# Performance work log

Measured on AMD Instinct MI355X. Metric: run time of the kernel, lower is better.

## Reference

```python
import jax, jax.numpy as jnp
import numpy as np

D_MODEL = 1024

def setup_inputs() -> dict:
    key = jax.random.key(0)
    kx, kq, kk, kv, ko = jax.random.split(key, 5)
    B, S, D = 8, 2048, D_MODEL
    scale = 1.0 / np.sqrt(D)
    x = jax.random.normal(kx, (B, S, D), dtype=jnp.float32)
    # nn.Linear weights are [out, in]; y = x @ W.T
    Wq = jax.random.normal(kq, (D, D), dtype=jnp.float32) * scale
    Wk = jax.random.normal(kk, (D, D), dtype=jnp.float32) * scale
    Wv = jax.random.normal(kv, (D, D), dtype=jnp.float32) * scale
    Wo = jax.random.normal(ko, (D, D), dtype=jnp.float32) * scale
    return {"x": x, "Wq": Wq, "Wk": Wk, "Wv": Wv, "Wo": Wo}

def reference(x, Wq, Wk, Wv, Wo):
    # Single-head self-attention, dropout in eval mode (identity).
    d_model = x.shape[-1]
    q = jnp.einsum('bsd,ed->bse', x, Wq)
    k = jnp.einsum('bsd,ed->bse', x, Wk)
    v = jnp.einsum('bsd,ed->bse', x, Wv)
    scores = jnp.einsum('bqe,bke->bqk', q, k) / jnp.sqrt(jnp.float32(d_model))
    attn = jax.nn.softmax(scores, axis=-1)
    weighted = jnp.einsum('bqk,bke->bqe', attn, v)
    return jnp.einsum('bqe,oe->bqo', weighted, Wo)
```

## Files before the change

kernel.cpp:

```cpp
#include <hip/hip_runtime.h>
#include <hip/hip_bf16.h>
#include <stdint.h>

typedef short bf16x8 __attribute__((ext_vector_type(8)));
typedef float f32x4 __attribute__((ext_vector_type(4)));

__device__ __forceinline__ unsigned short f2bf(float x) {
  uint32_t u = __builtin_bit_cast(uint32_t, x);
  u += 0x7FFFu + ((u >> 16) & 1u);
  return (unsigned short)(u >> 16);
}
__device__ __forceinline__ float bf2f(unsigned short u) {
  uint32_t v = ((uint32_t)u) << 16;
  return __builtin_bit_cast(float, v);
}

__device__ __forceinline__ void gl2lds16(const void* g, void* l) {
  __builtin_amdgcn_global_load_lds(
      (const __attribute__((address_space(1))) unsigned int*)g,
      (__attribute__((address_space(3))) unsigned int*)l, 16, 0, 0);
}

__global__ __launch_bounds__(256) void cast_f32_bf16_k(
    const float* __restrict__ s, unsigned short* __restrict__ d, long n) {
  long i = ((long)blockIdx.x * 256 + threadIdx.x) * 8;
  if (i >= n) return;
  float4 a = *(const float4*)(s + i);
  float4 b = *(const float4*)(s + i + 4);
  bf16x8 o;
  o[0] = (short)f2bf(a.x); o[1] = (short)f2bf(a.y);
  o[2] = (short)f2bf(a.z); o[3] = (short)f2bf(a.w);
  o[4] = (short)f2bf(b.x); o[5] = (short)f2bf(b.y);
  o[6] = (short)f2bf(b.z); o[7] = (short)f2bf(b.w);
  *(bf16x8*)(d + i) = o;
}

__global__ __launch_bounds__(256) void cast4_f32_bf16_k(
    const float* __restrict__ s0, const float* __restrict__ s1,
    const float* __restrict__ s2, const float* __restrict__ s3,
    unsigned short* __restrict__ d, long n) {
  const float* s = blockIdx.z == 0 ? s0 : blockIdx.z == 1 ? s1 : blockIdx.z == 2 ? s2 : s3;
  long i = ((long)blockIdx.x * 256 + threadIdx.x) * 8;
  if (i >= n) return;
  float4 a = *(const float4*)(s + i);
  float4 b = *(const float4*)(s + i + 4);
  bf16x8 o;
  o[0] = (short)f2bf(a.x); o[1] = (short)f2bf(a.y);
  o[2] = (short)f2bf(a.z); o[3] = (short)f2bf(a.w);
  o[4] = (short)f2bf(b.x); o[5] = (short)f2bf(b.y);
  o[6] = (short)f2bf(b.z); o[7] = (short)f2bf(b.w);
  *(bf16x8*)(d + blockIdx.z * n + i) = o;
}

template <typename OutT, bool FUSEQKV>
__global__ __launch_bounds__(512, 2) void gemm_bt8(
    const unsigned short* __restrict__ A, const unsigned short* __restrict__ B,
    OutT* __restrict__ C, int M, int N, int K,
    long sA, long sB, long sC, float alpha) {
  extern __shared__ __align__(16) char smem[];
  const int bz = blockIdx.z;
  const int gx = gridDim.x;
  const int nwg = gx * gridDim.y;
  const int idx = blockIdx.y * gx + blockIdx.x;
  const int wg = (idx & 7) * (nwg >> 3) + (idx >> 3);
  const int bm = wg / gx, bn = wg % gx;

  const int tid = threadIdx.x, lane = tid & 63, wave = tid >> 6;
  const int wm = wave >> 2, wn = wave & 3;

  const char* Ac = (const char*)(A + (long)bz * sA + (long)bm * 256 * K);
  const char* Bc = (const char*)(B + (long)bz * sB + (long)bn * 256 * K);
  C += (long)bz * sC;
  const long ld = (long)K * 2;

  const int sr = tid >> 3;
  const int scol = (((tid & 7) ^ ((tid >> 3) & 7)) << 4);

  auto stageChunk = [&](int buf, int op, int c, const char* gbase, int ktb) {
    char* reg = smem + ((buf * 2 + op) << 15);
    gl2lds16(gbase + (long)(sr + c * 64) * ld + (ktb + scol),
             reg + c * 8192 + tid * 16);
  };

  const int colx0 = ((lane >> 4) << 4) ^ ((lane & 7) << 4);
  const int colx1 = (64 | ((lane >> 4) << 4)) ^ ((lane & 7) << 4);
  const int rbA = (wm * 128 + (lane & 15)) * 128;
  const int rbB = (wn * 64 + (lane & 15)) * 128;

  f32x4 acc[8][4] = {};
  bf16x8 a0[4], a1[4], b0[4], b1[4];

  auto rdA = [&](bf16x8* dst, const char* reg, int g, int colx) {
#pragma unroll
    for (int m = 0; m < 4; ++m)
      dst[m] = *(const bf16x8*)(reg + rbA + g * (64 * 128) + m * (16 * 128) + colx);
  };
  auto rdB = [&](bf16x8* dst, const char* reg, int colx) {
#pragma unroll
    for (int n = 0; n < 4; ++n)
      dst[n] = *(const bf16x8*)(reg + rbB + n * (16 * 128) + colx);
  };
  auto mfma16 = [&](const bf16x8* af, const bf16x8* bf_, int g) {
    __builtin_amdgcn_s_setprio(1);
#pragma unroll
    for (int m = 0; m < 4; ++m)
#pragma unroll
      for (int n = 0; n < 4; ++n)
        acc[g * 4 + m][n] = __builtin_amdgcn_mfma_f32_16x16x32_bf16(
            af[m], bf_[n], acc[g * 4 + m][n], 0, 0, 0);
    __builtin_amdgcn_s_setprio(0);
    __builtin_amdgcn_sched_barrier(0);
  };

#pragma unroll
  for (int c = 0; c < 4; ++c) stageChunk(0, 0, c, Ac, 0);
#pragma unroll
  for (int c = 0; c < 4; ++c) stageChunk(0, 1, c, Bc, 0);
  asm volatile("s_waitcnt vmcnt(0)" ::: "memory");
  __builtin_amdgcn_s_barrier();
  rdA(a0, smem, 0, colx0);
  rdB(b0, smem + (1 << 15), colx0);

  const int nt = K >> 6;
  for (int t = 0; t < nt; ++t) {
    const int b = t & 1;
    const bool pf = (t + 1 < nt);
    const int ktb = (t + 1) << 7;
    const char* regA0 = smem + ((b * 2 + 0) << 15);
    const char* regB0 = smem + ((b * 2 + 1) << 15);
    const char* regA1 = smem + (((b ^ 1) * 2 + 0) << 15);
    const char* regB1 = smem + (((b ^ 1) * 2 + 1) << 15);

    if (pf) {
#pragma unroll
      for (int c = 0; c < 4; ++c) stageChunk(b ^ 1, 0, c, Ac, ktb);
    }
    rdA(a1, regA0, 1, colx0);
    asm volatile("s_waitcnt lgkmcnt(4)" ::: "memory");
    __builtin_amdgcn_sched_barrier(0);
    mfma16(a0, b0, 0);
    __builtin_amdgcn_s_barrier();

    if (pf) {
#pragma unroll
      for (int c = 0; c < 4; ++c) stageChunk(b ^ 1, 1, c, Bc, ktb);
    }
    rdA(a0, regA0, 0, colx1);
    rdB(b1, regB0, colx1);
    asm volatile("s_waitcnt lgkmcnt(8)" ::: "memory");
    __builtin_amdgcn_sched_barrier(0);
    mfma16(a1, b0, 1);
    __builtin_amdgcn_s_barrier();

    rdA(a1, regA0, 1, colx1);
    asm volatile("s_waitcnt lgkmcnt(4)" ::: "memory");
    __builtin_amdgcn_sched_barrier(0);
    mfma16(a0, b1, 0);
    __builtin_amdgcn_s_barrier();

    if (pf) {
      asm volatile("s_waitcnt vmcnt(0)" ::: "memory");
      __builtin_amdgcn_s_barrier();
      rdA(a0, regA1, 0, colx0);
      rdB(b0, regB1, colx0);
      asm volatile("s_waitcnt lgkmcnt(8)" ::: "memory");
    } else {
      asm volatile("s_waitcnt lgkmcnt(0)" ::: "memory");
    }
    __builtin_amdgcn_sched_barrier(0);
    mfma16(a1, b1, 1);
    __builtin_amdgcn_s_barrier();
  }

  const long row0 = (long)bm * 256 + wm * 128 + (lane >> 4) * 4;
  const int col0 = bn * 256 + wn * 64 + (lane & 15);
  if constexpr (FUSEQKV) {
    const int tensor = bn >> 2;
    unsigned short* dst = (unsigned short*)C + ((long)tensor << 24);
    const int colb0 = col0 - (tensor << 10);
#pragma unroll
    for (int m = 0; m < 8; ++m) {
#pragma unroll
      for (int n = 0; n < 4; ++n) {
        if (tensor < 2) {
#pragma unroll
          for (int r = 0; r < 4; ++r)
            dst[(row0 + m * 16 + r) * 1024 + colb0 + n * 16] = f2bf(acc[m][n][r]);
        } else {
          long row = row0 + m * 16;
          long base = ((row >> 11) << 21) + ((long)(colb0 + n * 16) << 11) + (row & 2047);
          ushort4 st;
          st.x = f2bf(acc[m][n][0]); st.y = f2bf(acc[m][n][1]);
          st.z = f2bf(acc[m][n][2]); st.w = f2bf(acc[m][n][3]);
          *(ushort4*)(dst + base) = st;
        }
      }
    }
  } else {
#pragma unroll
    for (int m = 0; m < 8; ++m) {
#pragma unroll
      for (int n = 0; n < 4; ++n) {
#pragma unroll
        for (int r = 0; r < 4; ++r) {
          long row = row0 + m * 16 + r;
          int col = col0 + n * 16;
          float v = acc[m][n][r] * alpha;
          if constexpr (sizeof(OutT) == 2)
            C[row * (long)N + col] = (OutT)f2bf(v);
          else
            C[row * (long)N + col] = v;
        }
      }
    }
  }
}

__global__ __launch_bounds__(256) void softmax_inplace(unsigned short* __restrict__ s, int C) {
  __shared__ float red[8];
  long row = blockIdx.x;
  unsigned short* p = s + row * (long)C;
  int tid = threadIdx.x, lane = tid & 63, w = tid >> 6;
  bf16x8 raw = *(const bf16x8*)(p + tid * 8);
  float v[8];
  float mx = -3.4e38f;
#pragma unroll
  for (int j = 0; j < 8; ++j) { v[j] = bf2f((unsigned short)raw[j]); mx = fmaxf(mx, v[j]); }
#pragma unroll
  for (int o = 32; o > 0; o >>= 1) mx = fmaxf(mx, __shfl_xor(mx, o));
  if (lane == 0) red[w] = mx;
  __syncthreads();
  mx = fmaxf(fmaxf(red[0], red[1]), fmaxf(red[2], red[3]));
  float sum = 0.f;
#pragma unroll
  for (int j = 0; j < 8; ++j) { v[j] = __expf(v[j] - mx); sum += v[j]; }
#pragma unroll
  for (int o = 32; o > 0; o >>= 1) sum += __shfl_xor(sum, o);
  if (lane == 0) red[4 + w] = sum;
  __syncthreads();
  float inv = 1.f / (red[4] + red[5] + red[6] + red[7]);
  bf16x8 o8;
#pragma unroll
  for (int j = 0; j < 8; ++j) o8[j] = (short)f2bf(v[j] * inv);
  *(bf16x8*)(p + tid * 8) = o8;
}

extern "C" void kernel_launch(void* const* d_in, const int* in_sizes, int n_in,
                              void* d_out, int out_size, void* d_ws, size_t ws_size,
                              hipStream_t stream) {
  (void)in_sizes; (void)n_in; (void)out_size; (void)ws_size;
  const float* x  = (const float*)d_in[0];
  const float* Wq = (const float*)d_in[1];
  const float* Wk = (const float*)d_in[2];
  const float* Wv = (const float*)d_in[3];
  const float* Wo = (const float*)d_in[4];
  const int B = 8, S = 2048, D = 1024;
  const long MB = 1 << 20;
  char* w = (char*)d_ws;
  unsigned short* Wqb = (unsigned short*)(w + 0 * MB);
  unsigned short* Wob = (unsigned short*)(w + 6 * MB);
  unsigned short* xb  = (unsigned short*)(w + 8 * MB);
  unsigned short* qb  = (unsigned short*)(w + 40 * MB);
  unsigned short* kb  = (unsigned short*)(w + 72 * MB);
  unsigned short* vt  = (unsigned short*)(w + 104 * MB);
  unsigned short* wb  = xb;
  unsigned short* attn = (unsigned short*)d_out;
  float* out = (float*)d_out;

  long nx = (long)B * S * D;
  long nw = (long)D * D;

  const int LDSB = 131072;
  hipFuncSetAttribute((const void*)gemm_bt8<unsigned short, true>,
                      hipFuncAttributeMaxDynamicSharedMemorySize, LDSB);
  hipFuncSetAttribute((const void*)gemm_bt8<unsigned short, false>,
                      hipFuncAttributeMaxDynamicSharedMemorySize, LDSB);
  hipFuncSetAttribute((const void*)gemm_bt8<float, false>,
                      hipFuncAttributeMaxDynamicSharedMemorySize, LDSB);

  cast_f32_bf16_k<<<(int)(nx / 2048), 256, 0, stream>>>(x, xb, nx);
  dim3 gW((int)(nw / 2048), 1, 4);
  cast4_f32_bf16_k<<<gW, 256, 0, stream>>>(Wq, Wk, Wv, Wo, Wqb, nw);

  dim3 gF(3072 / 256, (B * S) / 256, 1);
  gemm_bt8<unsigned short, true><<<gF, 512, LDSB, stream>>>(
      xb, Wqb, qb, B * S, 3072, D, 0, 0, 0, 1.f);

  dim3 gS(S / 256, S / 256, B);
  gemm_bt8<unsigned short, false><<<gS, 512, LDSB, stream>>>(qb, kb, attn, S, S, D,
      (long)S * D, (long)S * D, (long)S * S, 0.03125f);

  softmax_inplace<<<B * S, 256, 0, stream>>>(attn, S);

  dim3 gPV(D / 256, S / 256, B);
  gemm_bt8<unsigned short, false><<<gPV, 512, LDSB, stream>>>(attn, vt, wb, S, D, S,
      (long)S * S, (long)D * S, (long)S * D, 1.f);

  dim3 gP(D / 256, (B * S) / 256, 1);
  gemm_bt8<float, false><<<gP, 512, LDSB, stream>>>(wb, Wob, out, B * S, D, D, 0, 0, 0, 1.f);
}
```

Baseline: 324.4 us.

## Restructure GEMM main loop into half-tile staged pipeline with interleaved prefetch

Reorganizes the 256x256 bf16 GEMM k-loop so shared memory is split into 16KB half-tiles per operand and buffer. Global-to-LDS loads of the next A and B halves are issued piecemeal inside the MFMA sub-steps, with vmcnt(4) waits instead of full drains. The loop is unrolled two k-tiles at a time, and each wave reads smaller A and B fragments per sub-step. The aim is to overlap global loads with MFMA more evenly and shorten stalls, at the cost of more barriers and finer-grained synchronization that is harder to get right.

```diff
diff --git a/kernel.cpp b/kernel.cpp
--- a/kernel.cpp
+++ b/kernel.cpp
@@ -73,103 +73,86 @@
   C += (long)bz * sC;
   const long ld = (long)K * 2;
 
-  const int sr = tid >> 3;
-  const int scol = (((tid & 7) ^ ((tid >> 3) & 7)) << 4);
-
-  auto stageChunk = [&](int buf, int op, int c, const char* gbase, int ktb) {
-    char* reg = smem + ((buf * 2 + op) << 15);
-    gl2lds16(gbase + (long)(sr + c * 64) * ld + (ktb + scol),
-             reg + c * 8192 + tid * 16);
+  const int sr8 = tid >> 3;
+  const int scolx = (((tid & 7) ^ ((tid >> 3) & 7)) << 4);
+
+  auto stageHalf = [&](int t, int op, int h, const char* gbase) {
+    char* reg = smem + (((((t & 1) << 1) | op) << 1 | h) << 14);
+    const long ktb = (long)t << 7;
+#pragma unroll
+    for (int c = 0; c < 2; ++c)
+      gl2lds16(gbase + (long)(h * 128 + c * 64 + sr8) * ld + ktb + scolx,
+               reg + c * 8192 + tid * 16);
   };
 
-  const int colx0 = ((lane >> 4) << 4) ^ ((lane & 7) << 4);
-  const int colx1 = (64 | ((lane >> 4) << 4)) ^ ((lane & 7) << 4);
-  const int rbA = (wm * 128 + (lane & 15)) * 128;
-  const int rbB = (wn * 64 + (lane & 15)) * 128;
+  const char* Areg[2] = { smem + ((0 << 2 | wm) << 14),
+                          smem + ((1 << 2 | wm) << 14) };
+  const char* Breg[2] = { smem + (((0 << 2) | 2 | (wn >> 1)) << 14),
+                          smem + (((1 << 2) | 2 | (wn >> 1)) << 14) };
+  const int cko[2] = { (((lane >> 4) << 4) ^ ((lane & 7) << 4)),
+                       ((64 | ((lane >> 4) << 4)) ^ ((lane & 7) << 4)) };
+  const int rowA0 = (lane & 15) * 128;
+  const int rowB0 = ((wn & 1) * 64 + (lane & 15)) * 128;
 
   f32x4 acc[8][4] = {};
-  bf16x8 a0[4], a1[4], b0[4], b1[4];
-
-  auto rdA = [&](bf16x8* dst, const char* reg, int g, int colx) {
-#pragma unroll
-    for (int m = 0; m < 4; ++m)
-      dst[m] = *(const bf16x8*)(reg + rbA + g * (64 * 128) + m * (16 * 128) + colx);
-  };
-  auto rdB = [&](bf16x8* dst, const char* reg, int colx) {
-#pragma unroll
-    for (int n = 0; n < 4; ++n)
-      dst[n] = *(const bf16x8*)(reg + rbB + n * (16 * 128) + colx);
-  };
-  auto mfma16 = [&](const bf16x8* af, const bf16x8* bf_, int g) {
-    __builtin_amdgcn_s_setprio(1);
-#pragma unroll
-    for (int m = 0; m < 4; ++m)
-#pragma unroll
-      for (int n = 0; n < 4; ++n)
-        acc[g * 4 + m][n] = __builtin_amdgcn_mfma_f32_16x16x32_bf16(
-            af[m], bf_[n], acc[g * 4 + m][n], 0, 0, 0);
-    __builtin_amdgcn_s_setprio(0);
-    __builtin_amdgcn_sched_barrier(0);
-  };
-
-#pragma unroll
-  for (int c = 0; c < 4; ++c) stageChunk(0, 0, c, Ac, 0);
-#pragma unroll
-  for (int c = 0; c < 4; ++c) stageChunk(0, 1, c, Bc, 0);
-  asm volatile("s_waitcnt vmcnt(0)" ::: "memory");
+
+  stageHalf(0, 1, 0, Bc); stageHalf(0, 1, 1, Bc);
+  stageHalf(0, 0, 0, Ac); stageHalf(0, 0, 1, Ac);
+  stageHalf(1, 1, 0, Bc); stageHalf(1, 1, 1, Bc);
+  asm volatile("s_waitcnt vmcnt(4)" ::: "memory");
   __builtin_amdgcn_s_barrier();
-  rdA(a0, smem, 0, colx0);
-  rdB(b0, smem + (1 << 15), colx0);
 
   const int nt = K >> 6;
-  for (int t = 0; t < nt; ++t) {
-    const int b = t & 1;
-    const bool pf = (t + 1 < nt);
-    const int ktb = (t + 1) << 7;
-    const char* regA0 = smem + ((b * 2 + 0) << 15);
-    const char* regB0 = smem + ((b * 2 + 1) << 15);
-    const char* regA1 = smem + (((b ^ 1) * 2 + 0) << 15);
-    const char* regB1 = smem + (((b ^ 1) * 2 + 1) << 15);
-
-    if (pf) {
-#pragma unroll
-      for (int c = 0; c < 4; ++c) stageChunk(b ^ 1, 0, c, Ac, ktb);
+  const int niter = nt >> 1;
+  for (int i = 0; i < niter; ++i) {
+    const int u = 2 * i;
+    const bool pf = (i + 1 < niter);
+#pragma unroll
+    for (int d = 0; d < 2; ++d) {
+      bf16x8 b[4][2];
+#pragma unroll
+      for (int mq = 0; mq < 4; ++mq) {
+        bf16x8 a[2][2];
+        if (mq == 0) {
+#pragma unroll
+          for (int n = 0; n < 4; ++n)
+#pragma unroll
+            for (int kh = 0; kh < 2; ++kh)
+              b[n][kh] = *(const bf16x8*)(Breg[d] + rowB0 + n * 2048 + cko[kh]);
+        }
+#pragma unroll
+        for (int j = 0; j < 2; ++j)
+#pragma unroll
+          for (int kh = 0; kh < 2; ++kh)
+            a[j][kh] = *(const bf16x8*)(Areg[d] + rowA0 + (mq * 2 + j) * 2048 + cko[kh]);
+        if (d == 0 && mq == 0) { stageHalf(u + 1, 0, 0, Ac); stageHalf(u + 1, 0, 1, Ac); }
+        if (d == 0 && mq == 1 && pf) stageHalf(u + 2, 1, 0, Bc);
+        if (d == 0 && mq == 2 && pf) stageHalf(u + 2, 1, 1, Bc);
+        if (d == 1 && mq == 0 && pf) { stageHalf(u + 2, 0, 0, Ac); stageHalf(u + 2, 0, 1, Ac); }
+        if (d == 1 && mq == 1 && pf) stageHalf(u + 3, 1, 0, Bc);
+        if (d == 1 && mq == 2 && pf) stageHalf(u + 3, 1, 1, Bc);
+        if (mq == 0) asm volatile("s_waitcnt lgkmcnt(8)" ::: "memory");
+        __builtin_amdgcn_s_barrier();
+        asm volatile("s_waitcnt lgkmcnt(0)" ::: "memory");
+        __builtin_amdgcn_sched_barrier(0);
+        __builtin_amdgcn_s_setprio(1);
+#pragma unroll
+        for (int kh = 0; kh < 2; ++kh)
+#pragma unroll
+          for (int j = 0; j < 2; ++j)
+#pragma unroll
+            for (int n = 0; n < 4; ++n)
+              acc[mq * 2 + j][n] = __builtin_amdgcn_mfma_f32_16x16x32_bf16(
+                  a[j][kh], b[n][kh], acc[mq * 2 + j][n], 0, 0, 0);
+        __builtin_amdgcn_s_setprio(0);
+        if (d == 0 && mq == 3) {
+          if (pf) asm volatile("s_waitcnt vmcnt(4)" ::: "memory");
+          else    asm volatile("s_waitcnt vmcnt(0)" ::: "memory");
+        }
+        if (d == 1 && mq == 3 && pf) asm volatile("s_waitcnt vmcnt(4)" ::: "memory");
+        __builtin_amdgcn_s_barrier();
+      }
     }
-    rdA(a1, regA0, 1, colx0);
-    asm volatile("s_waitcnt lgkmcnt(4)" ::: "memory");
-    __builtin_amdgcn_sched_barrier(0);
-    mfma16(a0, b0, 0);
-    __builtin_amdgcn_s_barrier();
-
-    if (pf) {
-#pragma unroll
-      for (int c = 0; c < 4; ++c) stageChunk(b ^ 1, 1, c, Bc, ktb);
-    }
-    rdA(a0, regA0, 0, colx1);
-    rdB(b1, regB0, colx1);
-    asm volatile("s_waitcnt lgkmcnt(8)" ::: "memory");
-    __builtin_amdgcn_sched_barrier(0);
-    mfma16(a1, b0, 1);
-    __builtin_amdgcn_s_barrier();
-
-    rdA(a1, regA0, 1, colx1);
-    asm volatile("s_waitcnt lgkmcnt(4)" ::: "memory");
-    __builtin_amdgcn_sched_barrier(0);
-    mfma16(a0, b1, 0);
-    __builtin_amdgcn_s_barrier();
-
-    if (pf) {
-      asm volatile("s_waitcnt vmcnt(0)" ::: "memory");
-      __builtin_amdgcn_s_barrier();
-      rdA(a0, regA1, 0, colx0);
-      rdB(b0, regB1, colx0);
-      asm volatile("s_waitcnt lgkmcnt(8)" ::: "memory");
-    } else {
-      asm volatile("s_waitcnt lgkmcnt(0)" ::: "memory");
-    }
-    __builtin_amdgcn_sched_barrier(0);
-    mfma16(a1, b1, 1);
-    __builtin_amdgcn_s_barrier();
   }
 
   const long row0 = (long)bm * 256 + wm * 128 + (lane >> 4) * 4;
```

Result: no change. 329.4 us (+1.5%).
